# Optimization experiments

Hardware: AMD Instinct MI355X
Metric: run time of the kernel (lower is better)

Reference implementation:

```python
import jax, jax.numpy as jnp
import numpy as np
import math

B, T, D, N = 4, 2048, 1024, 16
HD = D // N
SCALE = math.sqrt(D)  # source scales by sqrt(d_key) = sqrt(full model dim)
BIG = 1e9

def setup_inputs() -> dict:
    key = jax.random.key(0)
    ks = jax.random.split(key, 11)
    s = 1.0 / math.sqrt(D)
    return {
        "query": jax.random.normal(ks[0], (B, T, D), jnp.float32),
        "key": jax.random.normal(ks[1], (B, T, D), jnp.float32),
        "value": jax.random.normal(ks[2], (B, T, D), jnp.float32),
        "wq_w": jax.random.normal(ks[3], (D, D), jnp.float32) * s,
        "wq_b": jnp.zeros((D,), jnp.float32),
        "wk_w": jax.random.normal(ks[4], (D, D), jnp.float32) * s,
        "wk_b": jnp.zeros((D,), jnp.float32),
        "wv_w": jax.random.normal(ks[5], (D, D), jnp.float32) * s,
        "wv_b": jnp.zeros((D,), jnp.float32),
        "wo_w": jax.random.normal(ks[6], (D, D), jnp.float32) * s,
        "wo_b": jnp.zeros((D,), jnp.float32),
    }

def reference(query, key, value, wq_w, wq_b, wk_w, wk_b, wv_w, wv_b, wo_w, wo_b):
    # projections (torch Linear equiv; weights stored as (in,out))
    q = query @ wq_w + wq_b
    k = key @ wk_w + wk_b
    v = value @ wv_w + wv_b
    # split heads: (B,T,D) -> (B,N,T,HD)
    def split(x):
        return x.reshape(B, T, N, HD).transpose(0, 2, 1, 3)
    q, k, v = split(q), split(k), split(v)
    # dot products (source does elementwise mul+sum == einsum)
    scores = jnp.einsum('bnqd,bnkd->bnqk', q, k)
    # only_attend_front: subtract 1e9 on strict upper triangle
    tri = jnp.triu(jnp.ones((T, T), scores.dtype), 1) * BIG
    scores = scores - tri
    logits = scores / SCALE
    probs = jax.nn.softmax(logits, axis=-1)
    # zero rows where every position is masked (source trick)
    alive = ((scores <= -BIG / 2).sum(-1, keepdims=True) < T).astype(probs.dtype)
    probs = probs * alive
    out = jnp.einsum('bnqk,bnkd->bnqd', probs, v)  # (B,N,T,HD)
    out = out.transpose(0, 2, 1, 3).reshape(B, T, D)
    return out @ wo_w + wo_b
```

## Files before the change

### kernel.cpp

```cpp
#include <hip/hip_runtime.h>
#include <hip/hip_bf16.h>

#define BB 4
#define TT 2048
#define DD 1024
#define NHEAD 16
#define HDIM 64

typedef __bf16 v8bf __attribute__((ext_vector_type(8)));
typedef __bf16 v4bf __attribute__((ext_vector_type(4)));
typedef float  v4f  __attribute__((ext_vector_type(4)));

#define C2SCALE 0.04508422376f

__device__ __forceinline__ void gl2lds16(const void* g, void* l) {
  __builtin_amdgcn_global_load_lds(
      (__attribute__((address_space(1))) const void*)g,
      (__attribute__((address_space(3))) void*)l, 16, 0, 0);
}

__global__ __launch_bounds__(256) void prep(
    const float* __restrict__ qsrc, const float* __restrict__ ksrc,
    const float* __restrict__ vsrc,
    const float* __restrict__ w0, const float* __restrict__ w1,
    const float* __restrict__ w2, const float* __restrict__ w3,
    __bf16* __restrict__ qdst, __bf16* __restrict__ kdst,
    __bf16* __restrict__ vdst,
    __bf16* __restrict__ t0, __bf16* __restrict__ t1,
    __bf16* __restrict__ t2, __bf16* __restrict__ t3) {
  constexpr int STR = 72;
  __shared__ __bf16 sh[64 * STR];
  int bx = blockIdx.x, tid = threadIdx.x;
  if (bx < 12288) {
    const float* src = bx < 4096 ? qsrc : bx < 8192 ? ksrc : vsrc;
    __bf16* dst = bx < 4096 ? qdst : bx < 8192 ? kdst : vdst;
    int i = (bx & 4095) * 256 + tid;
    const float4* s = (const float4*)src + (size_t)i * 2;
    float4 f0 = s[0], f1 = s[1];
    v8bf v;
    v[0] = (__bf16)f0.x; v[1] = (__bf16)f0.y; v[2] = (__bf16)f0.z; v[3] = (__bf16)f0.w;
    v[4] = (__bf16)f1.x; v[5] = (__bf16)f1.y; v[6] = (__bf16)f1.z; v[7] = (__bf16)f1.w;
    *(v8bf*)(dst + (size_t)i * 8) = v;
  } else {
    int idx = bx - 12288;
    int z = idx >> 8;
    const float* W = z == 0 ? w0 : z == 1 ? w1 : z == 2 ? w2 : w3;
    __bf16* Wt = z == 0 ? t0 : z == 1 ? t1 : z == 2 ? t2 : t3;
    int n0 = (idx & 15) * 64, k0 = ((idx >> 4) & 15) * 64;
#pragma unroll
    for (int p = 0; p < 4; ++p) {
      int c = tid + p * 256;
      int r = c >> 4, off = (c & 15) * 4;
      float4 f = *(const float4*)(W + (size_t)(k0 + r) * DD + n0 + off);
      __bf16* d = &sh[r * STR + off];
      d[0] = (__bf16)f.x; d[1] = (__bf16)f.y; d[2] = (__bf16)f.z; d[3] = (__bf16)f.w;
    }
    __syncthreads();
#pragma unroll
    for (int p = 0; p < 2; ++p) {
      int c = tid + p * 256;
      int nr = c >> 3, koff = (c & 7) * 8;
      v8bf v;
#pragma unroll
      for (int j = 0; j < 8; ++j) v[j] = sh[(koff + j) * STR + nr];
      *(v8bf*)(Wt + (size_t)(n0 + nr) * DD + k0 + koff) = v;
    }
  }
}

template <int MODE>
__global__ __launch_bounds__(256) void gemm128(const __bf16* __restrict__ A,
                                               const __bf16* __restrict__ Wt,
                                               const float* __restrict__ bias,
                                               void* __restrict__ Cv,
                                               float scale) {
  __shared__ __bf16 ash[128 * 64];
  __shared__ __bf16 bsh[128 * 64];
  int tid = threadIdx.x, wave = tid >> 6, lane = tid & 63;
  int quad = lane >> 4, l15 = lane & 15;
  int n0 = blockIdx.x * 128, m0 = blockIdx.y * 128;
  int wm = (wave & 1) * 64, wn = (wave >> 1) * 64;
  v4f acc[4][4];
#pragma unroll
  for (int jm = 0; jm < 4; ++jm)
#pragma unroll
    for (int jn = 0; jn < 4; ++jn) acc[jm][jn] = (v4f){0.f, 0.f, 0.f, 0.f};

  for (int k0 = 0; k0 < DD; k0 += 64) {
    __syncthreads();
#pragma unroll
    for (int i = 0; i < 4; ++i) {
      int c = wave * 256 + i * 64 + lane;
      int row = c >> 3, g = (c & 7) ^ (row & 7);
      gl2lds16(A + (size_t)(m0 + row) * DD + k0 + g * 8, ash + wave * 2048 + i * 512);
      gl2lds16(Wt + (size_t)(n0 + row) * DD + k0 + g * 8, bsh + wave * 2048 + i * 512);
    }
    __syncthreads();
#pragma unroll
    for (int ks = 0; ks < 2; ++ks) {
      int sw = (((ks * 4 + quad) ^ (l15 & 7))) * 8;
      v8bf a[4], b[4];
#pragma unroll
      for (int jm = 0; jm < 4; ++jm) a[jm] = *(v8bf*)&ash[(wm + jm * 16 + l15) * 64 + sw];
#pragma unroll
      for (int jn = 0; jn < 4; ++jn) b[jn] = *(v8bf*)&bsh[(wn + jn * 16 + l15) * 64 + sw];
#pragma unroll
      for (int jm = 0; jm < 4; ++jm)
#pragma unroll
        for (int jn = 0; jn < 4; ++jn)
          acc[jm][jn] = __builtin_amdgcn_mfma_f32_16x16x32_bf16(a[jm], b[jn], acc[jm][jn], 0, 0, 0);
    }
  }
  if constexpr (MODE == 2) {
    __bf16* VT = (__bf16*)Cv;
    int b = m0 >> 11;
    int tbase = (m0 & 2047) + wm;
#pragma unroll
    for (int jn = 0; jn < 4; ++jn) {
      int col = n0 + wn + jn * 16 + l15;
      float bv = bias[col];
      __bf16* rowp = VT + ((size_t)(b * 16 + (col >> 6)) * 64 + (col & 63)) * TT;
#pragma unroll
      for (int jm = 0; jm < 4; ++jm) {
        v4bf o;
#pragma unroll
        for (int r = 0; r < 4; ++r) o[r] = (__bf16)(acc[jm][jn][r] + bv);
        *(v4bf*)(rowp + tbase + jm * 16 + quad * 4) = o;
      }
    }
  } else {
#pragma unroll
    for (int jn = 0; jn < 4; ++jn) {
      int col = n0 + wn + jn * 16 + l15;
      float bv = bias[col];
#pragma unroll
      for (int jm = 0; jm < 4; ++jm) {
#pragma unroll
        for (int r = 0; r < 4; ++r) {
          int row = m0 + wm + jm * 16 + quad * 4 + r;
          if constexpr (MODE == 0)
            ((__bf16*)Cv)[(size_t)row * DD + col] = (__bf16)((acc[jm][jn][r] + bv) * scale);
          else
            ((float*)Cv)[(size_t)row * DD + col] = acc[jm][jn][r] + bv;
        }
      }
    }
  }
}

__global__ __launch_bounds__(256) void attn_bal(const __bf16* __restrict__ Q,
                                                const __bf16* __restrict__ K,
                                                const __bf16* __restrict__ VT,
                                                __bf16* __restrict__ O) {
  __shared__ __bf16 ksh[64 * 64];
  __shared__ __bf16 vsh[64 * 64];
  __shared__ __bf16 psh[128 * 64];
  int tid = threadIdx.x, wave = tid >> 6, lane = tid & 63;
  int quad = lane >> 4, l15 = lane & 15;
  int swz = l15 & 7;
  int bh = blockIdx.y;
  int b = bh >> 4, h = bh & 15;
  const __bf16* Qb = Q + (size_t)(b * TT) * DD + h * HDIM;
  const __bf16* Kb = K + (size_t)(b * TT) * DD + h * HDIM;
  const __bf16* Vb = VT + (size_t)bh * HDIM * TT;
  __bf16* Ob = O + (size_t)(b * TT) * DD + h * HDIM;

  for (int phase = 0; phase < 2; ++phase) {
    int qi = phase ? 15 - (int)blockIdx.x : (int)blockIdx.x;
    int q0 = qi * 128;

#pragma unroll
    for (int i = 0; i < 4; ++i) {
      int c = wave * 256 + i * 64 + lane;
      int row = c >> 3, g = (c & 7) ^ (row & 7);
      gl2lds16(Qb + (size_t)(q0 + row) * DD + g * 8, psh + wave * 2048 + i * 512);
    }
    __builtin_amdgcn_s_waitcnt(0);

    v8bf qf[2][2];
#pragma unroll
    for (int set = 0; set < 2; ++set)
#pragma unroll
      for (int ks = 0; ks < 2; ++ks)
        qf[set][ks] = *(v8bf*)&psh[(wave * 32 + set * 16 + l15) * 64 + ((ks * 4 + quad) ^ swz) * 8];

    int qg[2] = {q0 + wave * 32 + l15, q0 + wave * 32 + 16 + l15};
    float lr[2] = {0.f, 0.f};
    v4f oacc[2][4];
#pragma unroll
    for (int set = 0; set < 2; ++set)
#pragma unroll
      for (int jm = 0; jm < 4; ++jm) oacc[set][jm] = (v4f){0.f, 0.f, 0.f, 0.f};

    int ktiles = 2 * qi + 2;
    for (int kt = 0; kt < ktiles; ++kt) {
      int k0 = kt * 64;
      __syncthreads();
#pragma unroll
      for (int i = 0; i < 2; ++i) {
        int c = wave * 128 + i * 64 + lane;
        int row = c >> 3, g = (c & 7) ^ (row & 7);
        gl2lds16(Kb + (size_t)(k0 + row) * DD + g * 8, ksh + wave * 1024 + i * 512);
        gl2lds16(Vb + (size_t)row * TT + k0 + g * 8, vsh + wave * 1024 + i * 512);
      }
      __syncthreads();

      v4f s[2][4];
#pragma unroll
      for (int set = 0; set < 2; ++set)
#pragma unroll
        for (int jf = 0; jf < 4; ++jf) s[set][jf] = (v4f){0.f, 0.f, 0.f, 0.f};
#pragma unroll
      for (int ks = 0; ks < 2; ++ks) {
        int sw = ((ks * 4 + quad) ^ swz) * 8;
#pragma unroll
        for (int jf = 0; jf < 4; ++jf) {
          v8bf kf = *(v8bf*)&ksh[(jf * 16 + l15) * 64 + sw];
          s[0][jf] = __builtin_amdgcn_mfma_f32_16x16x32_bf16(kf, qf[0][ks], s[0][jf], 0, 0, 0);
          s[1][jf] = __builtin_amdgcn_mfma_f32_16x16x32_bf16(kf, qf[1][ks], s[1][jf], 0, 0, 0);
        }
      }

      bool diag = (kt >= 2 * qi);
#pragma unroll
      for (int set = 0; set < 2; ++set) {
        int qrow = wave * 32 + set * 16 + l15;
        __bf16* prow = &psh[qrow * 64];
#pragma unroll
        for (int jf = 0; jf < 4; ++jf) {
          v4bf pk;
#pragma unroll
          for (int r = 0; r < 4; ++r) {
            float p = __builtin_amdgcn_exp2f(s[set][jf][r]);
            if (diag) {
              int kg = k0 + jf * 16 + quad * 4 + r;
              if (kg > qg[set]) p = 0.f;
            }
            lr[set] += p;
            pk[r] = (__bf16)p;
          }
          int chunk = jf * 2 + (quad >> 1);
          *(v4bf*)&prow[(chunk ^ swz) * 8 + (quad & 1) * 4] = pk;
        }
      }

#pragma unroll
      for (int ks = 0; ks < 2; ++ks) {
        int sw = ((ks * 4 + quad) ^ swz) * 8;
        v8bf pb0 = *(v8bf*)&psh[(wave * 32 + l15) * 64 + sw];
        v8bf pb1 = *(v8bf*)&psh[(wave * 32 + 16 + l15) * 64 + sw];
#pragma unroll
        for (int jm = 0; jm < 4; ++jm) {
          v8bf vf = *(v8bf*)&vsh[(jm * 16 + l15) * 64 + sw];
          oacc[0][jm] = __builtin_amdgcn_mfma_f32_16x16x32_bf16(vf, pb0, oacc[0][jm], 0, 0, 0);
          oacc[1][jm] = __builtin_amdgcn_mfma_f32_16x16x32_bf16(vf, pb1, oacc[1][jm], 0, 0, 0);
        }
      }
    }

#pragma unroll
    for (int set = 0; set < 2; ++set) {
      float l = lr[set];
      l += __shfl_xor(l, 16, 64);
      l += __shfl_xor(l, 32, 64);
      float inv = 1.0f / l;
      int q = q0 + wave * 32 + set * 16 + l15;
#pragma unroll
      for (int jm = 0; jm < 4; ++jm) {
        v4bf o;
#pragma unroll
        for (int r = 0; r < 4; ++r) o[r] = (__bf16)(oacc[set][jm][r] * inv);
        *(v4bf*)(Ob + (size_t)q * DD + jm * 16 + quad * 4) = o;
      }
    }
  }
}

extern "C" void kernel_launch(void* const* d_in, const int* in_sizes, int n_in,
                              void* d_out, int out_size, void* d_ws, size_t ws_size,
                              hipStream_t stream) {
  const float* query = (const float*)d_in[0];
  const float* key_  = (const float*)d_in[1];
  const float* value = (const float*)d_in[2];
  const float* wq_w = (const float*)d_in[3];
  const float* wq_b = (const float*)d_in[4];
  const float* wk_w = (const float*)d_in[5];
  const float* wk_b = (const float*)d_in[6];
  const float* wv_w = (const float*)d_in[7];
  const float* wv_b = (const float*)d_in[8];
  const float* wo_w = (const float*)d_in[9];
  const float* wo_b = (const float*)d_in[10];

  char* ws = (char*)d_ws;
  const size_t MB = (size_t)1 << 20;
  __bf16* wqT = (__bf16*)(ws + 0 * MB);
  __bf16* wkT = (__bf16*)(ws + 2 * MB);
  __bf16* wvT = (__bf16*)(ws + 4 * MB);
  __bf16* woT = (__bf16*)(ws + 6 * MB);
  __bf16* Qc  = (__bf16*)(ws + 8 * MB);
  __bf16* Kc  = (__bf16*)(ws + 24 * MB);
  __bf16* Vc  = (__bf16*)(ws + 40 * MB);
  __bf16* Qp  = (__bf16*)(ws + 56 * MB);
  __bf16* Kp  = (__bf16*)(ws + 8 * MB);
  __bf16* VTb = (__bf16*)(ws + 24 * MB);
  __bf16* Ab  = (__bf16*)(ws + 40 * MB);
  float* out = (float*)d_out;

  dim3 tb(256);
  prep<<<dim3(13312), tb, 0, stream>>>(query, key_, value, wq_w, wk_w, wv_w, wo_w,
                                       Qc, Kc, Vc, wqT, wkT, wvT, woT);
  gemm128<0><<<dim3(8, 64), tb, 0, stream>>>(Qc, wqT, wq_b, Qp, C2SCALE);
  gemm128<0><<<dim3(8, 64), tb, 0, stream>>>(Kc, wkT, wk_b, Kp, 1.0f);
  gemm128<2><<<dim3(8, 64), tb, 0, stream>>>(Vc, wvT, wv_b, VTb, 1.0f);
  attn_bal<<<dim3(8, 64), tb, 0, stream>>>(Qp, Kp, VTb, Ab);
  gemm128<1><<<dim3(8, 64), tb, 0, stream>>>(Ab, woT, wo_b, out, 1.0f);
}
```

Before: 343.5 us.

## Merge QKV projections into one launch and swizzle block-to-tile mapping

Replaces three separate projection GEMM launches with a single 3D-grid kernel that selects Q, K or V by blockIdx.z, moving K/V outputs to non-aliased workspace regions. It also remaps linear block IDs so groups of 8 blocks cover different row tiles with the same column tile, in both the GEMMs and attention. The aim is to cut launch overhead and tail idleness and to improve L2 reuse. The attention remap changes which heads run concurrently, which may reduce K/V sharing between neighbouring blocks, and the workspace footprint grows.

```diff
diff --git a/kernel.cpp b/kernel.cpp
--- a/kernel.cpp
+++ b/kernel.cpp
@@ -68,24 +68,13 @@
   }
 }
 
-template <int MODE>
-__global__ __launch_bounds__(256) void gemm128(const __bf16* __restrict__ A,
-                                               const __bf16* __restrict__ Wt,
-                                               const float* __restrict__ bias,
-                                               void* __restrict__ Cv,
-                                               float scale) {
-  __shared__ __bf16 ash[128 * 64];
-  __shared__ __bf16 bsh[128 * 64];
-  int tid = threadIdx.x, wave = tid >> 6, lane = tid & 63;
-  int quad = lane >> 4, l15 = lane & 15;
-  int n0 = blockIdx.x * 128, m0 = blockIdx.y * 128;
+__device__ __forceinline__ void gemm_core(const __bf16* __restrict__ A,
+                                          const __bf16* __restrict__ Wt,
+                                          int m0, int n0,
+                                          __bf16* ash, __bf16* bsh,
+                                          int wave, int lane, int quad, int l15,
+                                          v4f acc[4][4]) {
   int wm = (wave & 1) * 64, wn = (wave >> 1) * 64;
-  v4f acc[4][4];
-#pragma unroll
-  for (int jm = 0; jm < 4; ++jm)
-#pragma unroll
-    for (int jn = 0; jn < 4; ++jn) acc[jm][jn] = (v4f){0.f, 0.f, 0.f, 0.f};
-
   for (int k0 = 0; k0 < DD; k0 += 64) {
     __syncthreads();
 #pragma unroll
@@ -111,15 +100,50 @@
           acc[jm][jn] = __builtin_amdgcn_mfma_f32_16x16x32_bf16(a[jm], b[jn], acc[jm][jn], 0, 0, 0);
     }
   }
-  if constexpr (MODE == 2) {
-    __bf16* VT = (__bf16*)Cv;
+}
+
+__device__ __forceinline__ void swz_tiles(int& m0, int& n0) {
+  int lin = blockIdx.x + 8 * blockIdx.y;
+  int c = lin & 7, t = lin >> 3;
+  n0 = (t & 7) * 128;
+  m0 = (c + ((t >> 3) << 3)) * 128;
+}
+
+__global__ __launch_bounds__(256) void gemm_qkv(
+    const __bf16* __restrict__ Qc, const __bf16* __restrict__ Kc,
+    const __bf16* __restrict__ Vc,
+    const __bf16* __restrict__ wqT, const __bf16* __restrict__ wkT,
+    const __bf16* __restrict__ wvT,
+    const float* __restrict__ qb, const float* __restrict__ kb,
+    const float* __restrict__ vb,
+    __bf16* __restrict__ Qp, __bf16* __restrict__ Kp, __bf16* __restrict__ VTb) {
+  __shared__ __bf16 ash[128 * 64];
+  __shared__ __bf16 bsh[128 * 64];
+  int z = blockIdx.z;
+  const __bf16* A  = z == 0 ? Qc : z == 1 ? Kc : Vc;
+  const __bf16* Wt = z == 0 ? wqT : z == 1 ? wkT : wvT;
+  const float* bias = z == 0 ? qb : z == 1 ? kb : vb;
+  int tid = threadIdx.x, wave = tid >> 6, lane = tid & 63;
+  int quad = lane >> 4, l15 = lane & 15;
+  int m0, n0;
+  swz_tiles(m0, n0);
+  int wm = (wave & 1) * 64, wn = (wave >> 1) * 64;
+  v4f acc[4][4];
+#pragma unroll
+  for (int jm = 0; jm < 4; ++jm)
+#pragma unroll
+    for (int jn = 0; jn < 4; ++jn) acc[jm][jn] = (v4f){0.f, 0.f, 0.f, 0.f};
+
+  gemm_core(A, Wt, m0, n0, ash, bsh, wave, lane, quad, l15, acc);
+
+  if (z == 2) {
     int b = m0 >> 11;
     int tbase = (m0 & 2047) + wm;
 #pragma unroll
     for (int jn = 0; jn < 4; ++jn) {
       int col = n0 + wn + jn * 16 + l15;
       float bv = bias[col];
-      __bf16* rowp = VT + ((size_t)(b * 16 + (col >> 6)) * 64 + (col & 63)) * TT;
+      __bf16* rowp = VTb + ((size_t)(b * 16 + (col >> 6)) * 64 + (col & 63)) * TT;
 #pragma unroll
       for (int jm = 0; jm < 4; ++jm) {
         v4bf o;
@@ -129,6 +153,8 @@
       }
     }
   } else {
+    __bf16* C = z == 0 ? Qp : Kp;
+    float scale = z == 0 ? C2SCALE : 1.0f;
 #pragma unroll
     for (int jn = 0; jn < 4; ++jn) {
       int col = n0 + wn + jn * 16 + l15;
@@ -138,11 +164,42 @@
 #pragma unroll
         for (int r = 0; r < 4; ++r) {
           int row = m0 + wm + jm * 16 + quad * 4 + r;
-          if constexpr (MODE == 0)
-            ((__bf16*)Cv)[(size_t)row * DD + col] = (__bf16)((acc[jm][jn][r] + bv) * scale);
-          else
-            ((float*)Cv)[(size_t)row * DD + col] = acc[jm][jn][r] + bv;
+          C[(size_t)row * DD + col] = (__bf16)((acc[jm][jn][r] + bv) * scale);
         }
+      }
+    }
+  }
+}
+
+__global__ __launch_bounds__(256) void gemm_out(const __bf16* __restrict__ A,
+                                                const __bf16* __restrict__ Wt,
+                                                const float* __restrict__ bias,
+                                                float* __restrict__ C) {
+  __shared__ __bf16 ash[128 * 64];
+  __shared__ __bf16 bsh[128 * 64];
+  int tid = threadIdx.x, wave = tid >> 6, lane = tid & 63;
+  int quad = lane >> 4, l15 = lane & 15;
+  int m0, n0;
+  swz_tiles(m0, n0);
+  int wm = (wave & 1) * 64, wn = (wave >> 1) * 64;
+  v4f acc[4][4];
+#pragma unroll
+  for (int jm = 0; jm < 4; ++jm)
+#pragma unroll
+    for (int jn = 0; jn < 4; ++jn) acc[jm][jn] = (v4f){0.f, 0.f, 0.f, 0.f};
+
+  gemm_core(A, Wt, m0, n0, ash, bsh, wave, lane, quad, l15, acc);
+
+#pragma unroll
+  for (int jn = 0; jn < 4; ++jn) {
+    int col = n0 + wn + jn * 16 + l15;
+    float bv = bias[col];
+#pragma unroll
+    for (int jm = 0; jm < 4; ++jm) {
+#pragma unroll
+      for (int r = 0; r < 4; ++r) {
+        int row = m0 + wm + jm * 16 + quad * 4 + r;
+        C[(size_t)row * DD + col] = acc[jm][jn][r] + bv;
       }
     }
   }
@@ -158,7 +215,10 @@
   int tid = threadIdx.x, wave = tid >> 6, lane = tid & 63;
   int quad = lane >> 4, l15 = lane & 15;
   int swz = l15 & 7;
-  int bh = blockIdx.y;
+  int lin = blockIdx.x + 8 * blockIdx.y;
+  int c = lin & 7, t = lin >> 3;
+  int xq = t & 7;
+  int bh = c + ((t >> 3) << 3);
   int b = bh >> 4, h = bh & 15;
   const __bf16* Qb = Q + (size_t)(b * TT) * DD + h * HDIM;
   const __bf16* Kb = K + (size_t)(b * TT) * DD + h * HDIM;
@@ -166,13 +226,13 @@
   __bf16* Ob = O + (size_t)(b * TT) * DD + h * HDIM;
 
   for (int phase = 0; phase < 2; ++phase) {
-    int qi = phase ? 15 - (int)blockIdx.x : (int)blockIdx.x;
+    int qi = phase ? 15 - xq : xq;
     int q0 = qi * 128;
 
 #pragma unroll
     for (int i = 0; i < 4; ++i) {
-      int c = wave * 256 + i * 64 + lane;
-      int row = c >> 3, g = (c & 7) ^ (row & 7);
+      int cc = wave * 256 + i * 64 + lane;
+      int row = cc >> 3, g = (cc & 7) ^ (row & 7);
       gl2lds16(Qb + (size_t)(q0 + row) * DD + g * 8, psh + wave * 2048 + i * 512);
     }
     __builtin_amdgcn_s_waitcnt(0);
@@ -198,8 +258,8 @@
       __syncthreads();
 #pragma unroll
       for (int i = 0; i < 2; ++i) {
-        int c = wave * 128 + i * 64 + lane;
-        int row = c >> 3, g = (c & 7) ^ (row & 7);
+        int cc = wave * 128 + i * 64 + lane;
+        int row = cc >> 3, g = (cc & 7) ^ (row & 7);
         gl2lds16(Kb + (size_t)(k0 + row) * DD + g * 8, ksh + wave * 1024 + i * 512);
         gl2lds16(Vb + (size_t)row * TT + k0 + g * 8, vsh + wave * 1024 + i * 512);
       }
@@ -301,17 +361,16 @@
   __bf16* Kc  = (__bf16*)(ws + 24 * MB);
   __bf16* Vc  = (__bf16*)(ws + 40 * MB);
   __bf16* Qp  = (__bf16*)(ws + 56 * MB);
-  __bf16* Kp  = (__bf16*)(ws + 8 * MB);
-  __bf16* VTb = (__bf16*)(ws + 24 * MB);
-  __bf16* Ab  = (__bf16*)(ws + 40 * MB);
+  __bf16* Kp  = (__bf16*)(ws + 72 * MB);
+  __bf16* VTb = (__bf16*)(ws + 88 * MB);
+  __bf16* Ab  = (__bf16*)(ws + 8 * MB);
   float* out = (float*)d_out;
 
   dim3 tb(256);
   prep<<<dim3(13312), tb, 0, stream>>>(query, key_, value, wq_w, wk_w, wv_w, wo_w,
                                        Qc, Kc, Vc, wqT, wkT, wvT, woT);
-  gemm128<0><<<dim3(8, 64), tb, 0, stream>>>(Qc, wqT, wq_b, Qp, C2SCALE);
-  gemm128<0><<<dim3(8, 64), tb, 0, stream>>>(Kc, wkT, wk_b, Kp, 1.0f);
-  gemm128<2><<<dim3(8, 64), tb, 0, stream>>>(Vc, wvT, wv_b, VTb, 1.0f);
+  gemm_qkv<<<dim3(8, 64, 3), tb, 0, stream>>>(Qc, Kc, Vc, wqT, wkT, wvT,
+                                              wq_b, wk_b, wv_b, Qp, Kp, VTb);
   attn_bal<<<dim3(8, 64), tb, 0, stream>>>(Qp, Kp, VTb, Ab);
-  gemm128<1><<<dim3(8, 64), tb, 0, stream>>>(Ab, woT, wo_b, out, 1.0f);
-}
+  gemm_out<<<dim3(8, 64), tb, 0, stream>>>(Ab, woT, wo_b, out);
+}
```

After: 322.1 us. 1.07x faster.
